# Kernel tuning notes

Hardware: AMD Instinct MI355X
Metric: run time of the kernel (lower is better)

Reference implementation:

```python
import math
import jax, jax.numpy as jnp
import numpy as np

D_MODEL = 1024
N_HEADS = 16
HEAD_DIM = D_MODEL // N_HEADS
B, L = 1, 4096


def _slopes(n_heads):
    ratio = 2.0 ** (-8.0 / n_heads)
    return jnp.asarray([ratio ** (i + 1) for i in range(n_heads)], dtype=jnp.float32)


def setup_inputs() -> dict:
    key = jax.random.key(0)
    ks = jax.random.split(key, 5)
    scale = 1.0 / math.sqrt(D_MODEL)
    return {
        "x": jax.random.normal(ks[0], (B, L, D_MODEL), dtype=jnp.float32),
        "q_w": jax.random.normal(ks[1], (D_MODEL, D_MODEL), dtype=jnp.float32) * scale,
        "k_w": jax.random.normal(ks[2], (D_MODEL, D_MODEL), dtype=jnp.float32) * scale,
        "v_w": jax.random.normal(ks[3], (D_MODEL, D_MODEL), dtype=jnp.float32) * scale,
        "o_w": jax.random.normal(ks[4], (D_MODEL, D_MODEL), dtype=jnp.float32) * scale,
    }


def reference(x, q_w, k_w, v_w, o_w):
    b, l, _ = x.shape
    # projections -> [B, H, L, hd]
    def proj(w):
        return (x @ w).reshape(b, l, N_HEADS, HEAD_DIM).transpose(0, 2, 1, 3)
    q, k, v = proj(q_w), proj(k_w), proj(v_w)

    scale = math.sqrt(HEAD_DIM)
    scores = jnp.einsum("bhid,bhjd->bhij", q, k) / scale  # [B,H,L,L]

    pos = jnp.arange(l)
    distance = jnp.abs(pos[None, :] - pos[:, None]).astype(jnp.float32)  # [L,L]
    alibi = -distance[None, :, :] * _slopes(N_HEADS)[:, None, None]       # [H,L,L]
    scores = scores + alibi[None]

    causal = pos[None, :] <= pos[:, None]  # j <= i
    scores = jnp.where(causal[None, None], scores, -jnp.inf)

    attn = jax.nn.softmax(scores, axis=-1)
    out = jnp.einsum("bhij,bhjd->bhid", attn, v)
    out = out.transpose(0, 2, 1, 3).reshape(b, l, D_MODEL)
    return out @ o_w
```

## Files before the change

### kernel.cpp

```cpp
#include <hip/hip_runtime.h>

#define L_SEQ 4096
#define DM    1024
#define NH    16
#define HD    64

typedef unsigned short ushort_t;
typedef __attribute__((ext_vector_type(8))) short bf16x8;
typedef __attribute__((ext_vector_type(4))) float f32x4;

__device__ inline unsigned short f2bf(float f) {
    union { float f; unsigned int u; } v; v.f = f;
    unsigned int r = v.u + 0x7fffu + ((v.u >> 16) & 1u);
    return (unsigned short)(r >> 16);
}

__device__ inline unsigned cvt_pk_bf16(float lo, float hi) {
    unsigned w;
    asm("v_cvt_pk_bf16_f32 %0, %1, %2" : "=v"(w) : "v"(lo), "v"(hi));
    return w;
}

__device__ inline void load_lds16(const ushort_t* g, ushort_t* l) {
    __builtin_amdgcn_global_load_lds(
        (const __attribute__((address_space(1))) unsigned int*)g,
        (__attribute__((address_space(3))) unsigned int*)l, 16, 0, 0);
}

__device__ inline bool detect_f32(const ushort_t* xraw) {
    __shared__ int s_flag;
    const int t = threadIdx.x;
    if (t < 64) {
        unsigned e = (xraw[2 * t] >> 7) & 0xFFu;
        unsigned long long m = __ballot(e >= 0x88u);
        if (t == 0) s_flag = (__popcll(m) >= 8) ? 1 : 0;
    }
    __syncthreads();
    return s_flag != 0;
}

__global__ __launch_bounds__(256) void convert_all(const void* __restrict__ xv,
                                                   const void* __restrict__ w0,
                                                   const void* __restrict__ w1,
                                                   const void* __restrict__ w2,
                                                   const void* __restrict__ w3,
                                                   ushort_t* __restrict__ xb,
                                                   ushort_t* __restrict__ wT) {
    bool f32 = detect_f32((const ushort_t*)xv);
    const int z = blockIdx.z;
    const int t = threadIdx.x;

    if (z == 4) {
        const int B0 = (blockIdx.y * 16 + blockIdx.x) * 16384;
        #pragma unroll
        for (int it = 0; it < 8; ++it) {
            const int i = B0 + it * 2048 + t * 8;
            if (f32) {
                const float* xf = (const float*)xv;
                float4 v0 = *(const float4*)(xf + i);
                float4 v1 = *(const float4*)(xf + i + 4);
                uint4 u;
                u.x = cvt_pk_bf16(v0.x, v0.y);
                u.y = cvt_pk_bf16(v0.z, v0.w);
                u.z = cvt_pk_bf16(v1.x, v1.y);
                u.w = cvt_pk_bf16(v1.z, v1.w);
                *(uint4*)(xb + i) = u;
            } else {
                *(uint4*)(xb + i) = *(const uint4*)((const ushort_t*)xv + i);
            }
        }
        return;
    }

    const void* w = (z == 0) ? w0 : (z == 1) ? w1 : (z == 2) ? w2 : w3;
    ushort_t* out = wT + (size_t)z * (DM * DM);
    __shared__ ushort_t T[64][65];
    const int k0 = blockIdx.x * 64, n0 = blockIdx.y * 64;
    #pragma unroll
    for (int i = 0; i < 16; ++i) {
        int e = t + i * 256;
        int r = e >> 6, c = e & 63;
        T[r][c] = f32 ? f2bf(((const float*)w)[(size_t)(k0 + r) * DM + n0 + c])
                      : ((const ushort_t*)w)[(size_t)(k0 + r) * DM + n0 + c];
    }
    __syncthreads();
    #pragma unroll
    for (int i = 0; i < 16; ++i) {
        int e = t + i * 256;
        int d = e >> 6, l = e & 63;
        out[(size_t)(n0 + d) * DM + k0 + l] = T[l][d];
    }
}

__device__ inline void gemm128_body(const ushort_t* __restrict__ A,
                                    const ushort_t* __restrict__ Bt,
                                    void* __restrict__ Cv, int cmode,
                                    int m0, int n0) {
    constexpr int K = 1024, NOUT = 1024;
    __shared__ ushort_t As[128 * 64];
    __shared__ ushort_t Bs[128 * 64];

    const int t = threadIdx.x, lane = t & 63, wave = t >> 6;
    const int l15 = lane & 15, quad = lane >> 4;
    const int mw = (wave >> 1) * 64, nw = (wave & 1) * 64;
    const int srow = lane >> 3;
    const int sgr  = (lane & 7) ^ (lane >> 3);
    const int swz  = l15 & 7;

    f32x4 acc[4][4] = {};

    for (int k0 = 0; k0 < K; k0 += 64) {
        #pragma unroll
        for (int i = 0; i < 4; ++i) {
            const int j = wave * 4 + i;
            load_lds16(A  + (size_t)(m0 + 8 * j + srow) * K + k0 + sgr * 8,
                       &As[8 * j * 64]);
            load_lds16(Bt + (size_t)(n0 + 8 * j + srow) * K + k0 + sgr * 8,
                       &Bs[8 * j * 64]);
        }
        __syncthreads();

        #pragma unroll
        for (int kt = 0; kt < 2; ++kt) {
            bf16x8 af[4], bf[4];
            #pragma unroll
            for (int i = 0; i < 4; ++i) {
                af[i] = *(const bf16x8*)&As[(mw + i * 16 + l15) * 64
                                            + (((kt * 4 + quad) ^ swz) * 8)];
                bf[i] = *(const bf16x8*)&Bs[(nw + i * 16 + l15) * 64
                                            + (((kt * 4 + quad) ^ swz) * 8)];
            }
            #pragma unroll
            for (int mt = 0; mt < 4; ++mt)
                #pragma unroll
                for (int nt = 0; nt < 4; ++nt)
                    acc[mt][nt] = __builtin_amdgcn_mfma_f32_16x16x32_bf16(
                        af[mt], bf[nt], acc[mt][nt], 0, 0, 0);
        }
        __syncthreads();
    }

    if (cmode == 2) {
        ushort_t* Vt = (ushort_t*)Cv;
        #pragma unroll
        for (int mt = 0; mt < 4; ++mt)
            #pragma unroll
            for (int nt = 0; nt < 4; ++nt) {
                int col  = n0 + nw + nt * 16 + l15;
                int row0 = m0 + mw + mt * 16 + quad * 4;
                ushort_t pk[4] = {f2bf(acc[mt][nt][0]), f2bf(acc[mt][nt][1]),
                                  f2bf(acc[mt][nt][2]), f2bf(acc[mt][nt][3])};
                *(uint2*)&Vt[(size_t)col * L_SEQ + row0] = *(const uint2*)pk;
            }
        return;
    }

    const int odd = lane & 1;
    #pragma unroll
    for (int mtp = 0; mtp < 2; ++mtp)
        #pragma unroll
        for (int nt = 0; nt < 4; ++nt)
            #pragma unroll
            for (int r = 0; r < 4; ++r) {
                float zA = acc[2 * mtp][nt][r];
                float zB = acc[2 * mtp + 1][nt][r];
                float send = odd ? zA : zB;
                float got  = __shfl_xor(send, 1);
                const int row = m0 + mw + (2 * mtp + odd) * 16 + quad * 4 + r;
                const int col = n0 + nw + nt * 16 + (l15 & ~1);
                if (cmode == 1) {
                    float2 w2 = odd ? make_float2(got, zB) : make_float2(zA, got);
                    *(float2*)((float*)Cv + (size_t)row * NOUT + col) = w2;
                } else {
                    float lo = odd ? got : zA;
                    float hi = odd ? zB  : got;
                    unsigned w = cvt_pk_bf16(lo, hi);
                    *(unsigned*)((ushort_t*)Cv + (size_t)row * NOUT + col) = w;
                }
            }
}

__global__ __launch_bounds__(256) void qkv128(const ushort_t* __restrict__ xb,
                                              const ushort_t* __restrict__ wT,
                                              ushort_t* Qp, ushort_t* Kp, ushort_t* Vt) {
    const int b = blockIdx.x;
    const int n0 = (b & 7) * 128, m0 = ((b >> 3) & 31) * 128, z = b >> 8;
    const ushort_t* Bt = wT + (size_t)z * (DM * DM);
    if (z == 0)      gemm128_body(xb, Bt, Qp, 0, m0, n0);
    else if (z == 1) gemm128_body(xb, Bt, Kp, 0, m0, n0);
    else             gemm128_body(xb, Bt, Vt, 2, m0, n0);
}

__global__ __launch_bounds__(256) void ogemm128(const void* __restrict__ xdet,
                                                const ushort_t* __restrict__ An,
                                                const ushort_t* __restrict__ woT,
                                                void* __restrict__ C) {
    bool f32 = detect_f32((const ushort_t*)xdet);
    const int b = blockIdx.x;
    const int n0 = (b & 7) * 128, m0 = (b >> 3) * 128;
    gemm128_body(An, woT, C, f32 ? 1 : 0, m0, n0);
}

__global__ __launch_bounds__(256) void attn_kernel(const ushort_t* __restrict__ Q,
                                                   const ushort_t* __restrict__ Kp,
                                                   const ushort_t* __restrict__ Vt,
                                                   ushort_t* __restrict__ O) {
    __shared__ ushort_t Ks[2][128 * 64];
    __shared__ ushort_t Vs[2][64 * 128];
    __shared__ ushort_t Pt[64 * 128];

    const int b    = blockIdx.x;
    const int h    = 2 * (b & 7) + ((b >> 3) & 1);
    const int bx   = b >> 4;
    const int t    = threadIdx.x;
    const int lane = t & 63, wave = t >> 6;
    const int l15  = lane & 15, quad = lane >> 4;
    const float LOG2E  = 1.44269504f;
    const float slope2 = exp2f(-0.5f * (float)(h + 1)) * LOG2E;
    const float c0     = 0.125f * LOG2E;
    const float qd4f   = (float)(quad * 4);

    const int krow = lane >> 3, kgr = (lane & 7) ^ (lane >> 3);
    const int vsub = lane >> 4;
    const int swz = l15 & 7;

    auto stage_load = [&](int buf, int kv0) {
        #pragma unroll
        for (int i = 0; i < 4; ++i) {
            const int j = wave * 4 + i;
            const int r = 8 * j + krow;
            load_lds16(Kp + (size_t)(kv0 + r) * DM + h * HD + kgr * 8,
                       &Ks[buf][8 * j * 64]);
        }
        #pragma unroll
        for (int i = 0; i < 4; ++i) {
            const int j = wave * 4 + i;
            const int d = 4 * j + vsub;
            const int g = (lane & 15) ^ (4 * (j & 1) + vsub);
            load_lds16(Vt + (size_t)(h * HD + d) * L_SEQ + kv0 + g * 8,
                       &Vs[buf][4 * j * 128]);
        }
    };

    int par = 0;
    stage_load(0, 0);

    #pragma unroll
    for (int half = 0; half < 2; ++half) {
        const int qb = half ? bx : (63 - bx);
        const int q0 = qb * 64;
        const int qg = q0 + wave * 16 + l15;
        const float qf = (float)qg;

        bf16x8 bq[2];
        #pragma unroll
        for (int kt = 0; kt < 2; ++kt)
            bq[kt] = *(const bf16x8*)(Q + (size_t)qg * DM + h * HD + kt * 32 + quad * 8);

        f32x4 acc_o[4] = {};
        float m2 = -1e30f, l_r = 0.f;

        const int nst = (qb + 2) >> 1;
        for (int s = 0; s < nst; ++s) {
            const int kv0 = s * 128;
            __syncthreads();

            const int nkv0 = (s + 1 < nst) ? (s + 1) * 128 : 0;
            stage_load(par ^ 1, nkv0);

            f32x4 sacc[8];
            #pragma unroll
            for (int mt = 0; mt < 8; ++mt) sacc[mt] = (f32x4){0.f, 0.f, 0.f, 0.f};
            #pragma unroll
            for (int kt = 0; kt < 2; ++kt)
                #pragma unroll
                for (int mt = 0; mt < 8; ++mt) {
                    bf16x8 a = *(const bf16x8*)&Ks[par][(mt * 16 + l15) * 64
                                                        + (((kt * 4 + quad) ^ swz) * 8)];
                    sacc[mt] = __builtin_amdgcn_mfma_f32_16x16x32_bf16(a, bq[kt], sacc[mt], 0, 0, 0);
                }

            const bool diag = (kv0 + 128 > q0);
            const float off = slope2 * ((float)kv0 + qd4f - qf);
            #pragma unroll
            for (int mt = 0; mt < 8; ++mt)
                #pragma unroll
                for (int r = 0; r < 4; ++r) {
                    float kvl = (float)(mt * 16 + r);
                    float s2  = fmaf(sacc[mt][r], c0, fmaf(slope2, kvl, off));
                    if (diag) {
                        int kvg = kv0 + mt * 16 + quad * 4 + r;
                        s2 = (kvg <= qg) ? s2 : -1e30f;
                    }
                    sacc[mt][r] = s2;
                }

            float mx = sacc[0][0];
            #pragma unroll
            for (int mt = 0; mt < 8; ++mt)
                #pragma unroll
                for (int r = 0; r < 4; ++r) mx = fmaxf(mx, sacc[mt][r]);
            mx = fmaxf(mx, __shfl_xor(mx, 16));
            mx = fmaxf(mx, __shfl_xor(mx, 32));

            const bool noresc = __all(mx - m2 <= 8.0f) != 0;
            float alpha = 1.0f;
            if (!noresc) {
                float m_new = fmaxf(m2, mx);
                alpha = exp2f(m2 - m_new);
                m2 = m_new;
            }

            float rs = 0.f;
            #pragma unroll
            for (int mt = 0; mt < 8; ++mt)
                #pragma unroll
                for (int r = 0; r < 4; ++r) {
                    float p = exp2f(sacc[mt][r] - m2);
                    sacc[mt][r] = p;
                    rs += p;
                }
            rs += __shfl_xor(rs, 16);
            rs += __shfl_xor(rs, 32);
            l_r = l_r * alpha + rs;

            if (!noresc) {
                float alpha_row[4];
                #pragma unroll
                for (int r = 0; r < 4; ++r) alpha_row[r] = __shfl(alpha, quad * 4 + r);
                #pragma unroll
                for (int nt = 0; nt < 4; ++nt)
                    #pragma unroll
                    for (int r = 0; r < 4; ++r) acc_o[nt][r] *= alpha_row[r];
            }

            #pragma unroll
            for (int mt = 0; mt < 8; ++mt) {
                union { float f; unsigned u; } a0, a1, a2, a3;
                a0.f = sacc[mt][0]; a1.f = sacc[mt][1];
                a2.f = sacc[mt][2]; a3.f = sacc[mt][3];
                uint2 w;
                w.x = __builtin_amdgcn_perm(a1.u, a0.u, 0x07060302);
                w.y = __builtin_amdgcn_perm(a3.u, a2.u, 0x07060302);
                const int g = mt * 2 + (quad >> 1);
                *(uint2*)&Pt[(wave * 16 + l15) * 128
                             + ((g ^ swz) * 8 + (quad & 1) * 4)] = w;
            }
            __threadfence_block();

            #pragma unroll
            for (int kt = 0; kt < 4; ++kt) {
                bf16x8 a = *(const bf16x8*)&Pt[(wave * 16 + l15) * 128
                                               + (((kt * 4 + quad) ^ swz) * 8)];
                #pragma unroll
                for (int nt = 0; nt < 4; ++nt) {
                    bf16x8 bvv = *(const bf16x8*)&Vs[par][(nt * 16 + l15) * 128
                                                          + (((kt * 4 + quad) ^ swz) * 8)];
                    acc_o[nt] = __builtin_amdgcn_mfma_f32_16x16x32_bf16(a, bvv, acc_o[nt], 0, 0, 0);
                }
            }

            par ^= 1;
        }

        float linv[4];
        #pragma unroll
        for (int r = 0; r < 4; ++r) linv[r] = 1.0f / __shfl(l_r, quad * 4 + r);
        #pragma unroll
        for (int nt = 0; nt < 4; ++nt)
            #pragma unroll
            for (int r = 0; r < 4; ++r) {
                int row = q0 + wave * 16 + quad * 4 + r;
                O[(size_t)row * DM + h * HD + nt * 16 + l15] = f2bf(acc_o[nt][r] * linv[r]);
            }
    }
}

extern "C" void kernel_launch(void* const* d_in, const int* in_sizes, int n_in,
                              void* d_out, int out_size, void* d_ws, size_t ws_size,
                              hipStream_t stream) {
    const void* x  = d_in[0];
    const void* wq = d_in[1];
    const void* wk = d_in[2];
    const void* wv = d_in[3];
    const void* wo = d_in[4];

    const size_t SZ = (size_t)L_SEQ * DM;
    const size_t WZ = (size_t)DM * DM;
    ushort_t* xb = (ushort_t*)d_ws;
    ushort_t* wT = xb + SZ;
    ushort_t* Qp = wT + 4 * WZ;
    ushort_t* Kp = Qp + SZ;
    ushort_t* Vt = Kp + SZ;
    ushort_t* An = xb;

    convert_all<<<dim3(16, 16, 5), 256, 0, stream>>>(x, wq, wk, wv, wo, xb, wT);
    qkv128<<<768, 256, 0, stream>>>(xb, wT, Qp, Kp, Vt);
    attn_kernel<<<512, 256, 0, stream>>>(Qp, Kp, Vt, An);
    ogemm128<<<256, 256, 0, stream>>>(x, An, wT + 3 * WZ, d_out);
}
```

Before: 255.2 us.

## Split attention into one q-tile per block with 64-wide KV tiles

The attention kernel moves from blocks that each process a paired long and short query tile with 128-wide KV stages to one query tile per block (1024 blocks) with 64-wide KV stages. LDS use per block halves and launch_bounds asks for 4 blocks per CU, aiming for higher occupancy and better latency hiding. s_setprio is raised around the MFMA sections. The cost is losing the explicit pairing that balanced the causal triangle, twice as many KV iterations with their barriers, and reliance on the hardware scheduler to even out the unequal block lengths.

```diff
diff --git a/kernel.cpp b/kernel.cpp
--- a/kernel.cpp
+++ b/kernel.cpp
@@ -201,17 +201,17 @@
     gemm128_body(An, woT, C, f32 ? 1 : 0, m0, n0);
 }
 
-__global__ __launch_bounds__(256) void attn_kernel(const ushort_t* __restrict__ Q,
-                                                   const ushort_t* __restrict__ Kp,
-                                                   const ushort_t* __restrict__ Vt,
-                                                   ushort_t* __restrict__ O) {
-    __shared__ ushort_t Ks[2][128 * 64];
-    __shared__ ushort_t Vs[2][64 * 128];
-    __shared__ ushort_t Pt[64 * 128];
+__global__ __launch_bounds__(256, 4) void attn_kernel(const ushort_t* __restrict__ Q,
+                                                      const ushort_t* __restrict__ Kp,
+                                                      const ushort_t* __restrict__ Vt,
+                                                      ushort_t* __restrict__ O) {
+    __shared__ ushort_t Ks[2][64 * 64];
+    __shared__ ushort_t Vs[2][64 * 64];
+    __shared__ ushort_t Pt[64 * 64];
 
     const int b    = blockIdx.x;
     const int h    = 2 * (b & 7) + ((b >> 3) & 1);
-    const int bx   = b >> 4;
+    const int qb   = 63 - (b >> 4);
     const int t    = threadIdx.x;
     const int lane = t & 63, wave = t >> 6;
     const int l15  = lane & 15, quad = lane >> 4;
@@ -221,159 +221,155 @@
     const float qd4f   = (float)(quad * 4);
 
     const int krow = lane >> 3, kgr = (lane & 7) ^ (lane >> 3);
-    const int vsub = lane >> 4;
-    const int swz = l15 & 7;
+    const int swz  = l15 & 7;
 
     auto stage_load = [&](int buf, int kv0) {
         #pragma unroll
-        for (int i = 0; i < 4; ++i) {
-            const int j = wave * 4 + i;
-            const int r = 8 * j + krow;
-            load_lds16(Kp + (size_t)(kv0 + r) * DM + h * HD + kgr * 8,
+        for (int i = 0; i < 2; ++i) {
+            const int j = wave * 2 + i;
+            load_lds16(Kp + (size_t)(kv0 + 8 * j + krow) * DM + h * HD + kgr * 8,
                        &Ks[buf][8 * j * 64]);
         }
         #pragma unroll
-        for (int i = 0; i < 4; ++i) {
-            const int j = wave * 4 + i;
-            const int d = 4 * j + vsub;
-            const int g = (lane & 15) ^ (4 * (j & 1) + vsub);
-            load_lds16(Vt + (size_t)(h * HD + d) * L_SEQ + kv0 + g * 8,
-                       &Vs[buf][4 * j * 128]);
+        for (int i = 0; i < 2; ++i) {
+            const int j = wave * 2 + i;
+            load_lds16(Vt + (size_t)(h * HD + 8 * j + krow) * L_SEQ + kv0 + kgr * 8,
+                       &Vs[buf][8 * j * 64]);
         }
     };
 
     int par = 0;
     stage_load(0, 0);
 
-    #pragma unroll
-    for (int half = 0; half < 2; ++half) {
-        const int qb = half ? bx : (63 - bx);
-        const int q0 = qb * 64;
-        const int qg = q0 + wave * 16 + l15;
-        const float qf = (float)qg;
-
-        bf16x8 bq[2];
+    const int q0 = qb * 64;
+    const int qg = q0 + wave * 16 + l15;
+    const float qf = (float)qg;
+
+    bf16x8 bq[2];
+    #pragma unroll
+    for (int kt = 0; kt < 2; ++kt)
+        bq[kt] = *(const bf16x8*)(Q + (size_t)qg * DM + h * HD + kt * 32 + quad * 8);
+
+    f32x4 acc_o[4] = {};
+    float m2 = -1e30f, l_r = 0.f;
+
+    const int nst = qb + 1;
+    for (int s = 0; s < nst; ++s) {
+        const int kv0 = s * 64;
+        __syncthreads();
+
+        const int nkv0 = (s + 1 < nst) ? (s + 1) * 64 : 0;
+        stage_load(par ^ 1, nkv0);
+
+        f32x4 sacc[4];
+        #pragma unroll
+        for (int mt = 0; mt < 4; ++mt) sacc[mt] = (f32x4){0.f, 0.f, 0.f, 0.f};
+        __builtin_amdgcn_s_setprio(1);
         #pragma unroll
         for (int kt = 0; kt < 2; ++kt)
-            bq[kt] = *(const bf16x8*)(Q + (size_t)qg * DM + h * HD + kt * 32 + quad * 8);
-
-        f32x4 acc_o[4] = {};
-        float m2 = -1e30f, l_r = 0.f;
-
-        const int nst = (qb + 2) >> 1;
-        for (int s = 0; s < nst; ++s) {
-            const int kv0 = s * 128;
-            __syncthreads();
-
-            const int nkv0 = (s + 1 < nst) ? (s + 1) * 128 : 0;
-            stage_load(par ^ 1, nkv0);
-
-            f32x4 sacc[8];
-            #pragma unroll
-            for (int mt = 0; mt < 8; ++mt) sacc[mt] = (f32x4){0.f, 0.f, 0.f, 0.f};
-            #pragma unroll
-            for (int kt = 0; kt < 2; ++kt)
+            #pragma unroll
+            for (int mt = 0; mt < 4; ++mt) {
+                bf16x8 a = *(const bf16x8*)&Ks[par][(mt * 16 + l15) * 64
+                                                    + (((kt * 4 + quad) ^ swz) * 8)];
+                sacc[mt] = __builtin_amdgcn_mfma_f32_16x16x32_bf16(a, bq[kt], sacc[mt], 0, 0, 0);
+            }
+        __builtin_amdgcn_s_setprio(0);
+
+        const bool diag = (kv0 + 64 > q0);
+        const float off = slope2 * ((float)kv0 + qd4f - qf);
+        #pragma unroll
+        for (int mt = 0; mt < 4; ++mt)
+            #pragma unroll
+            for (int r = 0; r < 4; ++r) {
+                float kvl = (float)(mt * 16 + r);
+                float s2  = fmaf(sacc[mt][r], c0, fmaf(slope2, kvl, off));
+                if (diag) {
+                    int kvg = kv0 + mt * 16 + quad * 4 + r;
+                    s2 = (kvg <= qg) ? s2 : -1e30f;
+                }
+                sacc[mt][r] = s2;
+            }
+
+        float mt0 = fmaxf(fmaxf(sacc[0][0], sacc[0][1]), fmaxf(sacc[0][2], sacc[0][3]));
+        float mt1 = fmaxf(fmaxf(sacc[1][0], sacc[1][1]), fmaxf(sacc[1][2], sacc[1][3]));
+        float mt2 = fmaxf(fmaxf(sacc[2][0], sacc[2][1]), fmaxf(sacc[2][2], sacc[2][3]));
+        float mt3 = fmaxf(fmaxf(sacc[3][0], sacc[3][1]), fmaxf(sacc[3][2], sacc[3][3]));
+        float mx  = fmaxf(fmaxf(mt0, mt1), fmaxf(mt2, mt3));
+        mx = fmaxf(mx, __shfl_xor(mx, 16));
+        mx = fmaxf(mx, __shfl_xor(mx, 32));
+
+        const bool noresc = __all(mx - m2 <= 8.0f) != 0;
+        float alpha = 1.0f;
+        if (!noresc) {
+            float m_new = fmaxf(m2, mx);
+            alpha = exp2f(m2 - m_new);
+            m2 = m_new;
+        }
+
+        float rs = 0.f;
+        #pragma unroll
+        for (int mt = 0; mt < 4; ++mt)
+            #pragma unroll
+            for (int r = 0; r < 4; ++r) {
+                float p = exp2f(sacc[mt][r] - m2);
+                sacc[mt][r] = p;
+                rs += p;
+            }
+        rs += __shfl_xor(rs, 16);
+        rs += __shfl_xor(rs, 32);
+        l_r = l_r * alpha + rs;
+
+        if (!noresc) {
+            float alpha_row[4];
+            #pragma unroll
+            for (int r = 0; r < 4; ++r) alpha_row[r] = __shfl(alpha, quad * 4 + r);
+            #pragma unroll
+            for (int nt = 0; nt < 4; ++nt)
                 #pragma unroll
-                for (int mt = 0; mt < 8; ++mt) {
-                    bf16x8 a = *(const bf16x8*)&Ks[par][(mt * 16 + l15) * 64
-                                                        + (((kt * 4 + quad) ^ swz) * 8)];
-                    sacc[mt] = __builtin_amdgcn_mfma_f32_16x16x32_bf16(a, bq[kt], sacc[mt], 0, 0, 0);
-                }
-
-            const bool diag = (kv0 + 128 > q0);
-            const float off = slope2 * ((float)kv0 + qd4f - qf);
-            #pragma unroll
-            for (int mt = 0; mt < 8; ++mt)
-                #pragma unroll
-                for (int r = 0; r < 4; ++r) {
-                    float kvl = (float)(mt * 16 + r);
-                    float s2  = fmaf(sacc[mt][r], c0, fmaf(slope2, kvl, off));
-                    if (diag) {
-                        int kvg = kv0 + mt * 16 + quad * 4 + r;
-                        s2 = (kvg <= qg) ? s2 : -1e30f;
-                    }
-                    sacc[mt][r] = s2;
-                }
-
-            float mx = sacc[0][0];
-            #pragma unroll
-            for (int mt = 0; mt < 8; ++mt)
-                #pragma unroll
-                for (int r = 0; r < 4; ++r) mx = fmaxf(mx, sacc[mt][r]);
-            mx = fmaxf(mx, __shfl_xor(mx, 16));
-            mx = fmaxf(mx, __shfl_xor(mx, 32));
-
-            const bool noresc = __all(mx - m2 <= 8.0f) != 0;
-            float alpha = 1.0f;
-            if (!noresc) {
-                float m_new = fmaxf(m2, mx);
-                alpha = exp2f(m2 - m_new);
-                m2 = m_new;
-            }
-
-            float rs = 0.f;
-            #pragma unroll
-            for (int mt = 0; mt < 8; ++mt)
-                #pragma unroll
-                for (int r = 0; r < 4; ++r) {
-                    float p = exp2f(sacc[mt][r] - m2);
-                    sacc[mt][r] = p;
-                    rs += p;
-                }
-            rs += __shfl_xor(rs, 16);
-            rs += __shfl_xor(rs, 32);
-            l_r = l_r * alpha + rs;
-
-            if (!noresc) {
-                float alpha_row[4];
-                #pragma unroll
-                for (int r = 0; r < 4; ++r) alpha_row[r] = __shfl(alpha, quad * 4 + r);
-                #pragma unroll
-                for (int nt = 0; nt < 4; ++nt)
-                    #pragma unroll
-                    for (int r = 0; r < 4; ++r) acc_o[nt][r] *= alpha_row[r];
-            }
-
-            #pragma unroll
-            for (int mt = 0; mt < 8; ++mt) {
-                union { float f; unsigned u; } a0, a1, a2, a3;
-                a0.f = sacc[mt][0]; a1.f = sacc[mt][1];
-                a2.f = sacc[mt][2]; a3.f = sacc[mt][3];
-                uint2 w;
-                w.x = __builtin_amdgcn_perm(a1.u, a0.u, 0x07060302);
-                w.y = __builtin_amdgcn_perm(a3.u, a2.u, 0x07060302);
-                const int g = mt * 2 + (quad >> 1);
-                *(uint2*)&Pt[(wave * 16 + l15) * 128
-                             + ((g ^ swz) * 8 + (quad & 1) * 4)] = w;
-            }
-            __threadfence_block();
-
-            #pragma unroll
-            for (int kt = 0; kt < 4; ++kt) {
-                bf16x8 a = *(const bf16x8*)&Pt[(wave * 16 + l15) * 128
-                                               + (((kt * 4 + quad) ^ swz) * 8)];
-                #pragma unroll
-                for (int nt = 0; nt < 4; ++nt) {
-                    bf16x8 bvv = *(const bf16x8*)&Vs[par][(nt * 16 + l15) * 128
-                                                          + (((kt * 4 + quad) ^ swz) * 8)];
-                    acc_o[nt] = __builtin_amdgcn_mfma_f32_16x16x32_bf16(a, bvv, acc_o[nt], 0, 0, 0);
-                }
-            }
-
-            par ^= 1;
-        }
-
-        float linv[4];
-        #pragma unroll
-        for (int r = 0; r < 4; ++r) linv[r] = 1.0f / __shfl(l_r, quad * 4 + r);
-        #pragma unroll
-        for (int nt = 0; nt < 4; ++nt)
-            #pragma unroll
-            for (int r = 0; r < 4; ++r) {
-                int row = q0 + wave * 16 + quad * 4 + r;
-                O[(size_t)row * DM + h * HD + nt * 16 + l15] = f2bf(acc_o[nt][r] * linv[r]);
-            }
-    }
+                for (int r = 0; r < 4; ++r) acc_o[nt][r] *= alpha_row[r];
+        }
+
+        #pragma unroll
+        for (int mt = 0; mt < 4; ++mt) {
+            union { float f; unsigned u; } a0, a1, a2, a3;
+            a0.f = sacc[mt][0]; a1.f = sacc[mt][1];
+            a2.f = sacc[mt][2]; a3.f = sacc[mt][3];
+            uint2 w;
+            w.x = __builtin_amdgcn_perm(a1.u, a0.u, 0x07060302);
+            w.y = __builtin_amdgcn_perm(a3.u, a2.u, 0x07060302);
+            const int g = mt * 2 + (quad >> 1);
+            *(uint2*)&Pt[(wave * 16 + l15) * 64
+                         + ((g ^ swz) * 8 + (quad & 1) * 4)] = w;
+        }
+        __threadfence_block();
+
+        __builtin_amdgcn_s_setprio(1);
+        #pragma unroll
+        for (int kt = 0; kt < 2; ++kt) {
+            bf16x8 a = *(const bf16x8*)&Pt[(wave * 16 + l15) * 64
+                                           + (((kt * 4 + quad) ^ swz) * 8)];
+            #pragma unroll
+            for (int nt = 0; nt < 4; ++nt) {
+                bf16x8 bvv = *(const bf16x8*)&Vs[par][(nt * 16 + l15) * 64
+                                                      + (((kt * 4 + quad) ^ swz) * 8)];
+                acc_o[nt] = __builtin_amdgcn_mfma_f32_16x16x32_bf16(a, bvv, acc_o[nt], 0, 0, 0);
+            }
+        }
+        __builtin_amdgcn_s_setprio(0);
+
+        par ^= 1;
+    }
+
+    float linv[4];
+    #pragma unroll
+    for (int r = 0; r < 4; ++r) linv[r] = 1.0f / __shfl(l_r, quad * 4 + r);
+    #pragma unroll
+    for (int nt = 0; nt < 4; ++nt)
+        #pragma unroll
+        for (int r = 0; r < 4; ++r) {
+            int row = q0 + wave * 16 + quad * 4 + r;
+            O[(size_t)row * DM + h * HD + nt * 16 + l15] = f2bf(acc_o[nt][r] * linv[r]);
+        }
 }
 
 extern "C" void kernel_launch(void* const* d_in, const int* in_sizes, int n_in,
@@ -396,6 +392,6 @@
 
     convert_all<<<dim3(16, 16, 5), 256, 0, stream>>>(x, wq, wk, wv, wo, xb, wT);
     qkv128<<<768, 256, 0, stream>>>(xb, wT, Qp, Kp, Vt);
-    attn_kernel<<<512, 256, 0, stream>>>(Qp, Kp, Vt, An);
+    attn_kernel<<<1024, 256, 0, stream>>>(Qp, Kp, Vt, An);
     ogemm128<<<256, 256, 0, stream>>>(x, An, wT + 3 * WZ, d_out);
 }
```

Result: no change. 256.5 us (+0.5%).
